# Kernel optimization log

Measured on AMD Instinct MI355X. Metric: run time of the kernel, lower is better.

## Reference

```python
import jax, jax.numpy as jnp
import numpy as np

B, N, D, H = 8, 1024, 768, 12
HD = D // H
SCALE = HD ** -0.5

def setup_inputs() -> dict:
    key = jax.random.key(0)
    k1, k2, k3, k4 = jax.random.split(key, 4)
    x = jax.random.normal(k1, (B, N, D), dtype=jnp.float32)
    weight = jax.random.uniform(k2, (B, N), dtype=jnp.float32)
    W_qkv = jax.random.normal(k3, (D, 3 * D), dtype=jnp.float32) * (D ** -0.5)
    W_msa = jax.random.normal(k4, (D, D), dtype=jnp.float32) * (D ** -0.5)
    b_msa = jnp.zeros((D,), dtype=jnp.float32)
    return {"x": x, "weight": weight, "W_qkv": W_qkv, "W_msa": W_msa, "b_msa": b_msa}

def reference(x, weight, W_qkv, W_msa, b_msa):
    # QKV projection (no bias), then elementwise per-token gate
    qkv = jnp.einsum('bnd,de->bne', x, W_qkv)          # [B,N,3D]
    qkv = weight[:, :, None] * qkv
    qkv = qkv.reshape(B, N, 3, H, HD).transpose(2, 0, 3, 1, 4)  # [3,B,H,N,hd]
    q, k, v = qkv[0], qkv[1], qkv[2]
    A = jnp.einsum('bhnd,bhmd->bhnm', q, k) * SCALE    # [B,H,N,N]
    A = jax.nn.softmax(A, axis=-1)
    out = jnp.einsum('bhnm,bhmd->bhnd', A, v)          # [B,H,N,hd]
    out = out.transpose(0, 2, 1, 3).reshape(B, N, D)
    return jnp.einsum('bnd,de->bne', out, W_msa) + b_msa
```

## Files before the change

### kernel.cpp

```cpp
#include <hip/hip_runtime.h>
#include <hip/hip_bf16.h>


typedef __attribute__((ext_vector_type(8))) short bf8;
typedef __attribute__((ext_vector_type(4))) float f4;

#define QSCALE 0.1803368801111204f

static __device__ __forceinline__ short bf16_of(float f) {
    union { float f; unsigned u; } a; a.f = f;
    unsigned r = a.u + 0x7FFFu + ((a.u >> 16) & 1u);
    return (short)(r >> 16);
}

static __device__ __forceinline__ unsigned bfpk(float lo, float hi) {
    float2 t; t.x = lo; t.y = hi;
    __hip_bfloat162 b = __float22bfloat162_rn(t);
    union { __hip_bfloat162 b; unsigned u; } c; c.b = b;
    return c.u;
}

static __device__ __forceinline__ void async16(const short* g, short* l) {
    __builtin_amdgcn_global_load_lds(
        (const __attribute__((address_space(1))) void*)g,
        (__attribute__((address_space(3))) void*)l, 16, 0, 0);
}

__global__ __launch_bounds__(256) void k_cvt(const float* __restrict__ src,
                                             const float* __restrict__ gate,
                                             short* __restrict__ dst, int n8) {
    int i = blockIdx.x * 256 + threadIdx.x;
    if (i >= n8) return;
    const float g = gate[i / 96];
    const f4* sp = (const f4*)src;
    f4 a = sp[2 * i], b = sp[2 * i + 1];
    union { bf8 v; short h[8]; } o;
    o.h[0] = bf16_of(a[0] * g); o.h[1] = bf16_of(a[1] * g);
    o.h[2] = bf16_of(a[2] * g); o.h[3] = bf16_of(a[3] * g);
    o.h[4] = bf16_of(b[0] * g); o.h[5] = bf16_of(b[1] * g);
    o.h[6] = bf16_of(b[2] * g); o.h[7] = bf16_of(b[3] * g);
    ((bf8*)dst)[i] = o.v;
}

__global__ __launch_bounds__(256) void k_transpose(const float* __restrict__ w,
                                                   short* __restrict__ wt,
                                                   int K, int E) {
    __shared__ short t[64][65];
    const int k0 = blockIdx.y * 64, e0 = blockIdx.x * 64;
    const int tid = threadIdx.x;
#pragma unroll
    for (int p = 0; p < 16; ++p) {
        int idx = p * 256 + tid;
        int r = idx >> 6, c = idx & 63;
        t[r][c] = bf16_of(w[(k0 + r) * E + e0 + c]);
    }
    __syncthreads();
#pragma unroll
    for (int p = 0; p < 16; ++p) {
        int idx = p * 256 + tid;
        int r = idx >> 6, c = idx & 63;
        wt[(e0 + r) * K + k0 + c] = t[c][r];
    }
}

static __device__ __forceinline__ void gemm128(const short* __restrict__ gA,
                                               const short* __restrict__ gB,
                                               short* smem,
                                               f4 acc[4][4]) {
    const int tid = threadIdx.x, lane = tid & 63;
    const int l16 = lane & 15, quad = lane >> 4, rx = l16 & 7;
    const int wm = (tid >> 6) & 1, wn = tid >> 7;

    auto stage = [&](short* S, int k0) {
#pragma unroll
        for (int c = 0; c < 4; ++c) {
            int p = c * 256 + tid;
            int row = p >> 3, slot = p & 7;
            int gc = slot ^ (row & 7);
            async16(gA + row * 768 + k0 + gc * 8, S + p * 8);
            async16(gB + row * 768 + k0 + gc * 8, S + 8192 + p * 8);
        }
    };

    stage(smem, 0);
    for (int it = 0; it < 12; ++it) {
        __builtin_amdgcn_s_waitcnt(0);
        __syncthreads();
        short* Sc = smem + (it & 1) * 16384;
        if (it + 1 < 12) stage(smem + ((it + 1) & 1) * 16384, (it + 1) * 64);
        const short* As = Sc;
        const short* Bs = Sc + 8192;
#pragma unroll
        for (int ks = 0; ks < 2; ++ks) {
            bf8 af[4], bfr[4];
#pragma unroll
            for (int mt = 0; mt < 4; ++mt)
                af[mt] = *(const bf8*)(As + (wm * 64 + mt * 16 + l16) * 64 +
                                       (((ks * 4 + quad) ^ rx) * 8));
#pragma unroll
            for (int nt = 0; nt < 4; ++nt)
                bfr[nt] = *(const bf8*)(Bs + (wn * 64 + nt * 16 + l16) * 64 +
                                        (((ks * 4 + quad) ^ rx) * 8));
#pragma unroll
            for (int mt = 0; mt < 4; ++mt)
#pragma unroll
                for (int nt = 0; nt < 4; ++nt)
                    acc[mt][nt] = __builtin_amdgcn_mfma_f32_16x16x32_bf16(
                        af[mt], bfr[nt], acc[mt][nt], 0, 0, 0);
        }
    }
    __syncthreads();
}

__global__ __launch_bounds__(256) void k_gemm_qkv(
        const short* __restrict__ xb, const short* __restrict__ wtq,
        short* __restrict__ qb, short* __restrict__ kb, short* __restrict__ vt) {
    __shared__ short smem[32768];
    const int tid = threadIdx.x, lane = tid & 63;
    const int l16 = lane & 15, quad = lane >> 4;
    const int wm = (tid >> 6) & 1, wn = tid >> 7;
    const int m0 = blockIdx.y * 128, n0 = blockIdx.x * 128;
    f4 z = {0.f, 0.f, 0.f, 0.f};
    f4 acc[4][4] = {{z,z,z,z},{z,z,z,z},{z,z,z,z},{z,z,z,z}};
    gemm128(xb + m0 * 768, wtq + n0 * 768, smem, acc);

    const int which = n0 / 768;
    if (which < 2) {
#pragma unroll
        for (int mt = 0; mt < 4; ++mt) {
#pragma unroll
            for (int r = 0; r < 4; ++r) {
                const int row = m0 + wm * 64 + mt * 16 + quad * 4 + r;
                const int b = row >> 10, nn = row & 1023;
#pragma unroll
                for (int nt = 0; nt < 4; ++nt) {
                    const int ct = n0 + wn * 64 + nt * 16;
                    const int h = (ct - which * 768) >> 6;
                    const int hh = b * 12 + h;
                    const int hd = (ct & 63) + l16;
                    const float val = acc[mt][nt][r];
                    if (which == 0)
                        qb[(hh * 1024 + nn) * 64 + hd] = bf16_of(val * QSCALE);
                    else
                        kb[(hh * 1024 + nn) * 64 + hd] = bf16_of(val);
                }
            }
        }
    } else {
#pragma unroll
        for (int mt = 0; mt < 4; ++mt) {
#pragma unroll
            for (int r = 0; r < 4; ++r) {
                const int tok = wm * 64 + mt * 16 + quad * 4 + r;
#pragma unroll
                for (int nt = 0; nt < 4; ++nt) {
                    const int dim = wn * 64 + nt * 16 + l16;
                    smem[dim * 132 + tok] = bf16_of(acc[mt][nt][r]);
                }
            }
        }
        __syncthreads();
        const int b = m0 >> 10, nn0 = m0 & 1023;
#pragma unroll
        for (int ps = 0; ps < 8; ++ps) {
            const int row = ps * 16 + (tid >> 4);
            const int chunk = tid & 15;
            const int dg = (n0 - 1536) + row;
            const int h = dg >> 6, hd = dg & 63;
            bf8 val = *(const bf8*)(smem + row * 132 + chunk * 8);
            *(bf8*)(vt + ((b * 12 + h) * 64 + hd) * 1024 + nn0 + chunk * 8) = val;
        }
    }
}

__global__ __launch_bounds__(256) void k_gemm_final(
        const short* __restrict__ attn, const short* __restrict__ wtm,
        const float* __restrict__ bias, float* __restrict__ out) {
    __shared__ short smem[32768];
    const int lane = threadIdx.x & 63;
    const int l16 = lane & 15, quad = lane >> 4;
    const int wm = (threadIdx.x >> 6) & 1, wn = threadIdx.x >> 7;
    const int m0 = blockIdx.y * 128, n0 = blockIdx.x * 128;
    f4 z = {0.f, 0.f, 0.f, 0.f};
    f4 acc[4][4] = {{z,z,z,z},{z,z,z,z},{z,z,z,z},{z,z,z,z}};
    gemm128(attn + m0 * 768, wtm + n0 * 768, smem, acc);
#pragma unroll
    for (int mt = 0; mt < 4; ++mt) {
#pragma unroll
        for (int r = 0; r < 4; ++r) {
            const int row = m0 + wm * 64 + mt * 16 + quad * 4 + r;
#pragma unroll
            for (int nt = 0; nt < 4; ++nt) {
                const int e = n0 + wn * 64 + nt * 16 + l16;
                out[row * 768 + e] = acc[mt][nt][r] + bias[e];
            }
        }
    }
}

__global__ __launch_bounds__(512) void k_attn(const short* __restrict__ qb,
                                              const short* __restrict__ kb,
                                              const short* __restrict__ vt,
                                              short* __restrict__ attn) {
    __shared__ short Ks[2][4096];
    __shared__ short Vs[2][4096];
    const int tid = threadIdx.x, wave = tid >> 6, lane = tid & 63;
    const int l16 = lane & 15, quad = lane >> 4;
    const int bh = blockIdx.x;
    const int b = bh / 12, h = bh - b * 12;
    const int m_base = blockIdx.y * 128 + wave * 16;
    const short* qh = qb + bh * 65536;
    const short* kh = kb + bh * 65536;
    const short* vh = vt + bh * 65536;

    const int rA = ((l16 >> 2) << 3) + (l16 & 3);
    const int fK = (((rA >> 3) & 1) << 2) + (rA & 3);
    const int sK = (quad ^ fK) * 8;
    const int oAlo = rA * 64 + sK;
    const int oAhi = rA * 64 + (sK ^ 32);
    const int oBlo = oAlo + 256, oBhi = oAhi + 256;
    const int fV = (((l16 >> 3) & 1) << 2) + (l16 & 3);
    const int oV = l16 * 64 + ((quad ^ fV) * 8);

    const short* qp = qh + (m_base + l16) * 64 + quad * 8;
    bf8 qf0 = *(const bf8*)(qp);
    bf8 qf1 = *(const bf8*)(qp + 32);

    union { bf8 v; short h[8]; } onef;
#pragma unroll
    for (int i = 0; i < 8; ++i) onef.h[i] = (short)0x3F80;

    f4 z = {0.f, 0.f, 0.f, 0.f};
    f4 acc[4] = {z, z, z, z};
    f4 accl = z;

    auto stage = [&](int buf, int j0) {
        int idx = tid;
        int row = idx >> 3;
        int fr = (((row >> 3) & 1) << 2) + (row & 3);
        int gc = (idx & 7) ^ fr;
        async16(kh + (j0 + row) * 64 + gc * 8, Ks[buf] + idx * 8);
        async16(vh + row * 1024 + j0 + gc * 8, Vs[buf] + idx * 8);
    };

    stage(0, 0);
    int cur = 0;
    for (int it = 0; it < 16; ++it) {
        __builtin_amdgcn_s_waitcnt(0);
        __syncthreads();
        if (it + 1 < 16) stage(cur ^ 1, (it + 1) * 64);
        const short* Kc = Ks[cur];
        const short* Vc = Vs[cur];

#pragma unroll
        for (int jj = 0; jj < 64; jj += 32) {
            const short* kjj = Kc + jj * 64;
            bf8 kAlo = *(const bf8*)(kjj + oAlo);
            bf8 kAhi = *(const bf8*)(kjj + oAhi);
            bf8 kBlo = *(const bf8*)(kjj + oBlo);
            bf8 kBhi = *(const bf8*)(kjj + oBhi);

            f4 sA = z, sB = z;
            sA = __builtin_amdgcn_mfma_f32_16x16x32_bf16(kAlo, qf0, sA, 0, 0, 0);
            sA = __builtin_amdgcn_mfma_f32_16x16x32_bf16(kAhi, qf1, sA, 0, 0, 0);
            sB = __builtin_amdgcn_mfma_f32_16x16x32_bf16(kBlo, qf0, sB, 0, 0, 0);
            sB = __builtin_amdgcn_mfma_f32_16x16x32_bf16(kBhi, qf1, sB, 0, 0, 0);
            float a0 = __builtin_amdgcn_exp2f(sA[0]);
            float a1 = __builtin_amdgcn_exp2f(sA[1]);
            float a2 = __builtin_amdgcn_exp2f(sA[2]);
            float a3 = __builtin_amdgcn_exp2f(sA[3]);
            float b0 = __builtin_amdgcn_exp2f(sB[0]);
            float b1 = __builtin_amdgcn_exp2f(sB[1]);
            float b2 = __builtin_amdgcn_exp2f(sB[2]);
            float b3 = __builtin_amdgcn_exp2f(sB[3]);
            union { bf8 v; unsigned u[4]; } p;
            p.u[0] = bfpk(a0, a1); p.u[1] = bfpk(a2, a3);
            p.u[2] = bfpk(b0, b1); p.u[3] = bfpk(b2, b3);
            accl = __builtin_amdgcn_mfma_f32_16x16x32_bf16(
                onef.v, p.v, accl, 0, 0, 0);

#pragma unroll
            for (int dt = 0; dt < 4; ++dt) {
                bf8 vf = *(const bf8*)(Vc + dt * 1024 + (oV ^ (jj ? 32 : 0)));
                acc[dt] = __builtin_amdgcn_mfma_f32_16x16x32_bf16(
                    vf, p.v, acc[dt], 0, 0, 0);
            }
        }
        cur ^= 1;
    }

    const float inv = 1.f / accl[0];
    const int row = (b << 10) + m_base + l16;
    short* op = attn + row * 768 + h * 64 + quad * 4;
#pragma unroll
    for (int dt = 0; dt < 4; ++dt)
#pragma unroll
        for (int r = 0; r < 4; ++r)
            op[dt * 16 + r] = bf16_of(acc[dt][r] * inv);
}

extern "C" void kernel_launch(void* const* d_in, const int* in_sizes, int n_in,
                              void* d_out, int out_size, void* d_ws, size_t ws_size,
                              hipStream_t stream) {
    const float* x    = (const float*)d_in[0];
    const float* gate = (const float*)d_in[1];
    const float* Wqkv = (const float*)d_in[2];
    const float* Wmsa = (const float*)d_in[3];
    const float* bmsa = (const float*)d_in[4];
    float* out = (float*)d_out;

    char* ws = (char*)d_ws;
    short* xb  = (short*)(ws);
    short* wtq = (short*)(ws + 12582912);
    short* wtm = (short*)(ws + 16121856);
    short* qb  = (short*)(ws + 17301504);
    short* kb  = (short*)(ws + 29884416);
    short* vt  = (short*)(ws + 42467328);
    short* attn = xb;

    k_cvt<<<3072, 256, 0, stream>>>(x, gate, xb, 786432);
    k_transpose<<<dim3(36, 12), 256, 0, stream>>>(Wqkv, wtq, 768, 2304);
    k_transpose<<<dim3(12, 12), 256, 0, stream>>>(Wmsa, wtm, 768, 768);
    k_gemm_qkv<<<dim3(18, 64), 256, 0, stream>>>(xb, wtq, qb, kb, vt);
    k_attn<<<dim3(96, 8), 512, 0, stream>>>(qb, kb, vt, attn);
    k_gemm_final<<<dim3(6, 64), 256, 0, stream>>>(attn, wtm, bmsa, out);
}
```

Measured before the change: 185.0 us.

## Rewrite QKV GEMM as 256x256 tile, 8-wave, half-staged pipelined kernel

The QKV projection GEMM moves from 128x128 tiles with 4 waves to 256x256 tiles with 8 waves. The main loop is double-buffered at half-tile granularity, issuing async global-to-LDS loads between MFMA phases, with barriers and setprio to interleave loads and compute. The 1D grid uses a swizzled block mapping intended to improve L2 reuse. Larger tiles raise arithmetic intensity but cut the grid to 288 blocks, which may leave CUs unevenly loaded and increases register pressure.

```diff
diff --git a/kernel.cpp b/kernel.cpp
--- a/kernel.cpp
+++ b/kernel.cpp
@@ -112,25 +112,140 @@
     __syncthreads();
 }
 
-__global__ __launch_bounds__(256) void k_gemm_qkv(
+__global__ __launch_bounds__(512, 2) void k_gemm_qkv(
         const short* __restrict__ xb, const short* __restrict__ wtq,
         short* __restrict__ qb, short* __restrict__ kb, short* __restrict__ vt) {
-    __shared__ short smem[32768];
+    __shared__ short lds[65536];
     const int tid = threadIdx.x, lane = tid & 63;
-    const int l16 = lane & 15, quad = lane >> 4;
-    const int wm = (tid >> 6) & 1, wn = tid >> 7;
-    const int m0 = blockIdx.y * 128, n0 = blockIdx.x * 128;
+    const int l16 = lane & 15, quad = lane >> 4, rx = l16 & 7;
+    const int wv = tid >> 6, wm = wv >> 2, wn = wv & 3;
+
+    const int wg = blockIdx.x;
+    const int swz = (wg & 7) * 36 + (wg >> 3);
+    const int mI = swz / 9, nI = swz - mI * 9;
+    const int m0 = mI * 256, n0 = nI * 256;
+
+    const short* gA = xb + m0 * 768;
+    const short* gB = wtq + n0 * 768;
+
+    auto stageHalf = [&](int buf, int isB, int half, const short* gsrc, int k0) {
+        short* dst = lds + buf * 32768 + isB * 16384 + half * 8192;
+        const short* src = gsrc + half * 98304 + k0;
+#pragma unroll
+        for (int j = 0; j < 2; ++j) {
+            int p = j * 512 + tid;
+            int row = p >> 3;
+            int gc = (p & 7) ^ (row & 7);
+            async16(src + row * 768 + gc * 8, dst + p * 8);
+        }
+    };
+
     f4 z = {0.f, 0.f, 0.f, 0.f};
-    f4 acc[4][4] = {{z,z,z,z},{z,z,z,z},{z,z,z,z},{z,z,z,z}};
-    gemm128(xb + m0 * 768, wtq + n0 * 768, smem, acc);
-
-    const int which = n0 / 768;
+    f4 acc[8][4];
+#pragma unroll
+    for (int mt = 0; mt < 8; ++mt)
+#pragma unroll
+        for (int nt = 0; nt < 4; ++nt) acc[mt][nt] = z;
+
+    stageHalf(0, 0, 0, gA, 0); stageHalf(0, 0, 1, gA, 0);
+    stageHalf(0, 1, 0, gB, 0); stageHalf(0, 1, 1, gB, 0);
+    stageHalf(1, 1, 0, gB, 64); stageHalf(1, 1, 1, gB, 64);
+    asm volatile("s_waitcnt vmcnt(4)" ::: "memory");
+    __builtin_amdgcn_s_barrier();
+
+#pragma unroll 2
+    for (int t = 0; t < 12; ++t) {
+        const short* Ab = lds + (t & 1) * 32768;
+        const short* Bb = Ab + 16384;
+        bf8 af[4][2], bfr[4][2];
+
+        auto rdA = [&](int mt, int ks) {
+            return *(const bf8*)(Ab + (wm * 128 + mt * 16 + l16) * 64 +
+                                 (((ks * 4 + quad) ^ rx) << 3));
+        };
+        auto rdB = [&](int nt, int ks) {
+            return *(const bf8*)(Bb + (wn * 64 + nt * 16 + l16) * 64 +
+                                 (((ks * 4 + quad) ^ rx) << 3));
+        };
+
+#pragma unroll
+        for (int mt = 0; mt < 4; ++mt) { af[mt][0] = rdA(mt, 0); af[mt][1] = rdA(mt, 1); }
+#pragma unroll
+        for (int nt = 0; nt < 2; ++nt) { bfr[nt][0] = rdB(nt, 0); bfr[nt][1] = rdB(nt, 1); }
+        if (t < 11) stageHalf((t + 1) & 1, 0, 0, gA, (t + 1) * 64);
+        __builtin_amdgcn_s_barrier();
+        __builtin_amdgcn_s_setprio(1);
+#pragma unroll
+        for (int mt = 0; mt < 4; ++mt)
+#pragma unroll
+            for (int nt = 0; nt < 2; ++nt) {
+                acc[mt][nt] = __builtin_amdgcn_mfma_f32_16x16x32_bf16(
+                    af[mt][0], bfr[nt][0], acc[mt][nt], 0, 0, 0);
+                acc[mt][nt] = __builtin_amdgcn_mfma_f32_16x16x32_bf16(
+                    af[mt][1], bfr[nt][1], acc[mt][nt], 0, 0, 0);
+            }
+        __builtin_amdgcn_s_setprio(0);
+        __builtin_amdgcn_s_barrier();
+
+#pragma unroll
+        for (int nt = 2; nt < 4; ++nt) { bfr[nt][0] = rdB(nt, 0); bfr[nt][1] = rdB(nt, 1); }
+        if (t < 11) stageHalf((t + 1) & 1, 0, 1, gA, (t + 1) * 64);
+        __builtin_amdgcn_s_barrier();
+        __builtin_amdgcn_s_setprio(1);
+#pragma unroll
+        for (int mt = 0; mt < 4; ++mt)
+#pragma unroll
+            for (int nt = 2; nt < 4; ++nt) {
+                acc[mt][nt] = __builtin_amdgcn_mfma_f32_16x16x32_bf16(
+                    af[mt][0], bfr[nt][0], acc[mt][nt], 0, 0, 0);
+                acc[mt][nt] = __builtin_amdgcn_mfma_f32_16x16x32_bf16(
+                    af[mt][1], bfr[nt][1], acc[mt][nt], 0, 0, 0);
+            }
+        __builtin_amdgcn_s_setprio(0);
+        __builtin_amdgcn_s_barrier();
+
+#pragma unroll
+        for (int mt = 0; mt < 4; ++mt) { af[mt][0] = rdA(mt + 4, 0); af[mt][1] = rdA(mt + 4, 1); }
+        if (t < 10) stageHalf(t & 1, 1, 0, gB, (t + 2) * 64);
+        __builtin_amdgcn_s_barrier();
+        __builtin_amdgcn_s_setprio(1);
+#pragma unroll
+        for (int mt = 0; mt < 4; ++mt)
+#pragma unroll
+            for (int nt = 2; nt < 4; ++nt) {
+                acc[mt + 4][nt] = __builtin_amdgcn_mfma_f32_16x16x32_bf16(
+                    af[mt][0], bfr[nt][0], acc[mt + 4][nt], 0, 0, 0);
+                acc[mt + 4][nt] = __builtin_amdgcn_mfma_f32_16x16x32_bf16(
+                    af[mt][1], bfr[nt][1], acc[mt + 4][nt], 0, 0, 0);
+            }
+        __builtin_amdgcn_s_setprio(0);
+        __builtin_amdgcn_s_barrier();
+
+        if (t < 10) stageHalf(t & 1, 1, 1, gB, (t + 2) * 64);
+        __builtin_amdgcn_s_barrier();
+        __builtin_amdgcn_s_setprio(1);
+#pragma unroll
+        for (int mt = 0; mt < 4; ++mt)
+#pragma unroll
+            for (int nt = 0; nt < 2; ++nt) {
+                acc[mt + 4][nt] = __builtin_amdgcn_mfma_f32_16x16x32_bf16(
+                    af[mt][0], bfr[nt][0], acc[mt + 4][nt], 0, 0, 0);
+                acc[mt + 4][nt] = __builtin_amdgcn_mfma_f32_16x16x32_bf16(
+                    af[mt][1], bfr[nt][1], acc[mt + 4][nt], 0, 0, 0);
+            }
+        __builtin_amdgcn_s_setprio(0);
+        if (t < 10)       asm volatile("s_waitcnt vmcnt(4)" ::: "memory");
+        else if (t == 10) asm volatile("s_waitcnt vmcnt(0)" ::: "memory");
+        __builtin_amdgcn_s_barrier();
+    }
+
+    const int which = (n0 >= 1536) ? 2 : (n0 >= 768 ? 1 : 0);
     if (which < 2) {
 #pragma unroll
-        for (int mt = 0; mt < 4; ++mt) {
+        for (int mt = 0; mt < 8; ++mt) {
 #pragma unroll
             for (int r = 0; r < 4; ++r) {
-                const int row = m0 + wm * 64 + mt * 16 + quad * 4 + r;
+                const int row = m0 + wm * 128 + mt * 16 + quad * 4 + r;
                 const int b = row >> 10, nn = row & 1023;
 #pragma unroll
                 for (int nt = 0; nt < 4; ++nt) {
@@ -147,28 +262,33 @@
             }
         }
     } else {
-#pragma unroll
-        for (int mt = 0; mt < 4; ++mt) {
-#pragma unroll
-            for (int r = 0; r < 4; ++r) {
-                const int tok = wm * 64 + mt * 16 + quad * 4 + r;
-#pragma unroll
-                for (int nt = 0; nt < 4; ++nt) {
-                    const int dim = wn * 64 + nt * 16 + l16;
-                    smem[dim * 132 + tok] = bf16_of(acc[mt][nt][r]);
-                }
-            }
-        }
-        __syncthreads();
         const int b = m0 >> 10, nn0 = m0 & 1023;
-#pragma unroll
-        for (int ps = 0; ps < 8; ++ps) {
-            const int row = ps * 16 + (tid >> 4);
-            const int chunk = tid & 15;
-            const int dg = (n0 - 1536) + row;
-            const int h = dg >> 6, hd = dg & 63;
-            bf8 val = *(const bf8*)(smem + row * 132 + chunk * 8);
-            *(bf8*)(vt + ((b * 12 + h) * 64 + hd) * 1024 + nn0 + chunk * 8) = val;
+        const int dg0 = n0 - 1536;
+#pragma unroll
+        for (int ch = 0; ch < 2; ++ch) {
+            if ((wn >> 1) == ch) {
+#pragma unroll
+                for (int mt = 0; mt < 8; ++mt)
+#pragma unroll
+                    for (int nt = 0; nt < 4; ++nt)
+#pragma unroll
+                        for (int r = 0; r < 4; ++r) {
+                            const int rl = wm * 128 + mt * 16 + quad * 4 + r;
+                            const int cl = wn * 64 + nt * 16 + l16 - ch * 128;
+                            lds[cl * 264 + rl] = bf16_of(acc[mt][nt][r]);
+                        }
+            }
+            __syncthreads();
+#pragma unroll
+            for (int ph = 0; ph < 8; ++ph) {
+                const int idx = ph * 512 + tid;
+                const int cl = idx >> 5, ck = idx & 31;
+                const int dg = dg0 + ch * 128 + cl;
+                const int h = dg >> 6, hd = dg & 63;
+                bf8 valv = *(const bf8*)(lds + cl * 264 + ck * 8);
+                *(bf8*)(vt + ((b * 12 + h) * 64 + hd) * 1024 + nn0 + ck * 8) = valv;
+            }
+            __syncthreads();
         }
     }
 }
@@ -321,7 +441,7 @@
     k_cvt<<<3072, 256, 0, stream>>>(x, gate, xb, 786432);
     k_transpose<<<dim3(36, 12), 256, 0, stream>>>(Wqkv, wtq, 768, 2304);
     k_transpose<<<dim3(12, 12), 256, 0, stream>>>(Wmsa, wtm, 768, 768);
-    k_gemm_qkv<<<dim3(18, 64), 256, 0, stream>>>(xb, wtq, qb, kb, vt);
+    k_gemm_qkv<<<288, 512, 0, stream>>>(xb, wtq, qb, kb, vt);
     k_attn<<<dim3(96, 8), 512, 0, stream>>>(qb, kb, vt, attn);
     k_gemm_final<<<dim3(6, 64), 256, 0, stream>>>(attn, wtm, bmsa, out);
 }
```

Result: slower. 196.4 us (+6.2%).
